# Optimization experiments

Hardware: AMD Instinct MI355X
Metric: run time of the kernel (lower is better)

The kernel has to match this reference:

```python
import jax, jax.numpy as jnp
import numpy as np

B, L, D, H = 2, 2048, 1024, 16
NEG = -1.0e9


def setup_inputs() -> dict:
    key = jax.random.key(0)
    k1, k2, k3, k4 = jax.random.split(key, 4)
    query = jax.random.normal(k1, (B, L, D), dtype=jnp.float32)
    key_t = jax.random.normal(k2, (B, L, D), dtype=jnp.float32)
    value = jax.random.normal(k3, (B, L, D), dtype=jnp.float32)
    # Conv1D c_proj params: w ~ N(0, 0.02), b = 0   (nx=D -> nf=D)
    w_proj = 0.02 * jax.random.normal(k4, (D, D), dtype=jnp.float32)
    b_proj = jnp.zeros((D,), dtype=jnp.float32)
    return {"query": query, "key": key_t, "value": value,
            "w_proj": w_proj, "b_proj": b_proj, "n_head": H}


def reference(query, key, value, w_proj, b_proj, n_head):
    b, l, d = query.shape
    dh = d // n_head
    # split_heads -> [B, H, L, dh]
    q = query.reshape(b, l, n_head, dh).transpose(0, 2, 1, 3)
    k = key.reshape(b, l, n_head, dh).transpose(0, 2, 1, 3)
    v = value.reshape(b, l, n_head, dh).transpose(0, 2, 1, 3)
    # scores: [B, H, L, L], scaled by sqrt(head_dim) (v.size(-1) after split)
    w = jnp.einsum("bhqd,bhkd->bhqk", q, k) / jnp.sqrt(jnp.float32(dh))
    # one_dir_visible=True: multiplicative causal mask, w*m + (-1e9)*(1-m)
    m = jnp.tril(jnp.ones((l, l), dtype=w.dtype))[None, None]
    w = w * m + NEG * (1.0 - m)
    p = jax.nn.softmax(w, axis=-1)  # attn_dropout p=0 -> identity
    a = jnp.einsum("bhqk,bhkd->bhqd", p, v)  # [B, H, L, dh]
    # merge_heads -> [B, L, D]
    a = a.transpose(0, 2, 1, 3).reshape(b, l, d)
    # c_proj (Conv1D == dense): resid_dropout p=0 -> identity
    return a @ w_proj + b_proj
```

## Files before the change

kernel.cpp:

```cpp
#include <hip/hip_runtime.h>
#include <hip/hip_bf16.h>

constexpr int kB  = 2;
constexpr int kL  = 2048;
constexpr int kD  = 1024;
constexpr int kH  = 16;
constexpr int kDH = 64;
constexpr int kM  = kB * kL;

typedef _Float16 half8 __attribute__((ext_vector_type(8)));
typedef float    f32x4 __attribute__((ext_vector_type(4)));

constexpr size_t kKhOff = 0;
constexpr size_t kVtOff = 8388608;
constexpr size_t kAhOff = 16777216;
constexpr size_t kWtOff = 25165824;
constexpr size_t kWsNeed = 27262976;

__device__ __forceinline__ void load16_lds(const void* g, void* l) {
    __builtin_amdgcn_global_load_lds((__attribute__((address_space(1))) void*)(g),
                                     (__attribute__((address_space(3))) void*)(l),
                                     16, 0, 0);
}

__global__ __launch_bounds__(256) void conv_fused(const float* __restrict__ K,
                                                  const float* __restrict__ V,
                                                  const float* __restrict__ W,
                                                  _Float16* __restrict__ Kh,
                                                  _Float16* __restrict__ Vt,
                                                  _Float16* __restrict__ Wt) {
    __shared__ _Float16 Ts[64][65];
    const int t = threadIdx.x;
    const int bid = blockIdx.x;

    if (bid < 2048) {
        size_t i = ((size_t)bid * 256 + t) * 8;
        float4 f0 = *(const float4*)(K + i);
        float4 f1 = *(const float4*)(K + i + 4);
        half8 h;
        h[0] = (_Float16)f0.x; h[1] = (_Float16)f0.y; h[2] = (_Float16)f0.z; h[3] = (_Float16)f0.w;
        h[4] = (_Float16)f1.x; h[5] = (_Float16)f1.y; h[6] = (_Float16)f1.z; h[7] = (_Float16)f1.w;
        *(half8*)(Kh + i) = h;
    } else if (bid < 3072) {
        const int b2 = bid - 2048;
        const int lt = b2 & 31, h = (b2 >> 5) & 15, b = b2 >> 9;
        for (int p = 0; p < 16; ++p) {
            int i = p * 256 + t;
            int r = i >> 6, c = i & 63;
            Ts[r][c] = (_Float16)V[((size_t)(b * kL + lt * 64 + r)) * kD + h * kDH + c];
        }
        __syncthreads();
        for (int p = 0; p < 16; ++p) {
            int i = p * 256 + t;
            int r = i >> 6, c = i & 63;
            Vt[((size_t)(b * kH + h) * kDH + r) * kL + lt * 64 + c] = Ts[c][r];
        }
    } else {
        const int b3 = bid - 3072;
        const int nt = b3 & 15, kt = b3 >> 4;
        const int k0 = kt * 64, n0 = nt * 64;
        for (int p = 0; p < 16; ++p) {
            int i = p * 256 + t;
            int r = i >> 6, c = i & 63;
            Ts[r][c] = (_Float16)W[(size_t)(k0 + r) * kD + n0 + c];
        }
        __syncthreads();
        for (int p = 0; p < 16; ++p) {
            int i = p * 256 + t;
            int r = i >> 6, c = i & 63;
            Wt[(size_t)(n0 + r) * kD + k0 + c] = Ts[c][r];
        }
    }
}

__global__ __launch_bounds__(256, 4) void flash_kernel(const float* __restrict__ Q,
                                                       const _Float16* __restrict__ Kh,
                                                       const _Float16* __restrict__ Vt,
                                                       _Float16* __restrict__ Ah) {
    __shared__ __align__(16) _Float16 Ks[2][64 * 64];
    __shared__ __align__(16) _Float16 Vs[2][64 * 64];
    __shared__ __align__(16) _Float16 Ps[4][16 * 64];

    const int t = threadIdx.x;
    const int lane = t & 63, w = t >> 6;
    const int l15 = lane & 15, quad = lane >> 4;
    const int lhi = l15 >> 3, llo = l15 & 7;
    const int bid = blockIdx.x;
    const int bh = bid & 31;
    const int qt = 31 - (bid >> 5);
    const int b = bh >> 4, h = bh & 15;
    const int Tq = qt + 1;
    const int qrow0 = qt * 64 + w * 16;
    const size_t hoff = (size_t)h * kDH;

    const int srow = w * 16 + (lane >> 3);
    const int sj   = ((lane & 7) - (lane >> 3)) & 7;
    const _Float16* kgp = Kh + (size_t)(b * kL) * kD + hoff + sj * 8;
    const _Float16* vgp = Vt + (size_t)(bh * kDH) * kL + sj * 8;

    half8 aq[2];
    #pragma unroll
    for (int kc = 0; kc < 2; ++kc) {
        const float* qp = Q + (size_t)(b * kL + qrow0 + l15) * kD + hoff + kc * 32 + quad * 8;
        float4 f0 = *(const float4*)qp;
        float4 f1 = *(const float4*)(qp + 4);
        half8 hq;
        hq[0] = (_Float16)(f0.x * 0.125f); hq[1] = (_Float16)(f0.y * 0.125f);
        hq[2] = (_Float16)(f0.z * 0.125f); hq[3] = (_Float16)(f0.w * 0.125f);
        hq[4] = (_Float16)(f1.x * 0.125f); hq[5] = (_Float16)(f1.y * 0.125f);
        hq[6] = (_Float16)(f1.z * 0.125f); hq[7] = (_Float16)(f1.w * 0.125f);
        aq[kc] = hq;
    }

    half8 ones;
    #pragma unroll
    for (int i = 0; i < 8; ++i) ones[i] = (_Float16)1.0f;

    f32x4 o[4];
    f32x4 lsum = (f32x4){0.f, 0.f, 0.f, 0.f};
    #pragma unroll
    for (int nt = 0; nt < 4; ++nt) o[nt] = (f32x4){0.f, 0.f, 0.f, 0.f};

    _Float16* pp = Ps[w];

    constexpr float kLog2e = 1.4426950408889634f;
    constexpr float kBias  = -11.541560327111707f;

    load16_lds(kgp + (size_t)srow * kD,       &Ks[0][(w * 16) * 64]);
    load16_lds(kgp + (size_t)(srow + 8) * kD, &Ks[0][(w * 16 + 8) * 64]);
    load16_lds(vgp + (size_t)srow * kL,       &Vs[0][(w * 16) * 64]);
    load16_lds(vgp + (size_t)(srow + 8) * kL, &Vs[0][(w * 16 + 8) * 64]);

    for (int kt = 0; kt < Tq; ++kt) {
        const int cur = kt & 1;
        __syncthreads();

        if (kt + 1 < Tq) {
            const int kb1 = (kt + 1) * 64;
            load16_lds(kgp + (size_t)(kb1 + srow) * kD,     &Ks[cur ^ 1][(w * 16) * 64]);
            load16_lds(kgp + (size_t)(kb1 + srow + 8) * kD, &Ks[cur ^ 1][(w * 16 + 8) * 64]);
            load16_lds(vgp + (size_t)srow * kL + kb1,       &Vs[cur ^ 1][(w * 16) * 64]);
            load16_lds(vgp + (size_t)(srow + 8) * kL + kb1, &Vs[cur ^ 1][(w * 16 + 8) * 64]);
        }

        f32x4 s[4];
        #pragma unroll
        for (int nt = 0; nt < 4; ++nt) {
            s[nt] = (f32x4){0.f, 0.f, 0.f, 0.f};
            #pragma unroll
            for (int kc = 0; kc < 2; ++kc) {
                const int r = nt * 16 + l15;
                const int slot = (quad + 4 * kc + l15) & 7;
                half8 bk = *(half8*)&Ks[cur][r * 64 + slot * 8];
                s[nt] = __builtin_amdgcn_mfma_f32_16x16x32_f16(aq[kc], bk, s[nt], 0, 0, 0);
            }
        }

        if (kt == Tq - 1) {
            const int kb = kt * 64;
            const int row = qrow0 + quad * 4;
            #pragma unroll
            for (int nt = 0; nt < 4; ++nt)
                #pragma unroll
                for (int r = 0; r < 4; ++r)
                    if (kb + nt * 16 + l15 > row + r) s[nt][r] = -1.0e30f;
        }

        #pragma unroll
        for (int nt = 0; nt < 4; ++nt)
            #pragma unroll
            for (int r = 0; r < 4; ++r) {
                float p = exp2f(fmaf(s[nt][r], kLog2e, kBias));
                const int prow = quad * 4 + r;
                const int slot = (nt * 2 + lhi + prow) & 7;
                pp[prow * 64 + slot * 8 + llo] = (_Float16)p;
            }

        half8 ap[2];
        #pragma unroll
        for (int kc = 0; kc < 2; ++kc) {
            const int slot = (kc * 4 + quad + l15) & 7;
            ap[kc] = *(half8*)&pp[l15 * 64 + slot * 8];
        }

        #pragma unroll
        for (int nt = 0; nt < 4; ++nt)
            #pragma unroll
            for (int kc = 0; kc < 2; ++kc) {
                const int r = nt * 16 + l15;
                const int slot = (quad + 4 * kc + l15) & 7;
                half8 bv = *(half8*)&Vs[cur][r * 64 + slot * 8];
                o[nt] = __builtin_amdgcn_mfma_f32_16x16x32_f16(ap[kc], bv, o[nt], 0, 0, 0);
            }
        lsum = __builtin_amdgcn_mfma_f32_16x16x32_f16(ap[0], ones, lsum, 0, 0, 0);
        lsum = __builtin_amdgcn_mfma_f32_16x16x32_f16(ap[1], ones, lsum, 0, 0, 0);
    }

    const size_t orow = (size_t)(b * kL + qrow0 + quad * 4);
    #pragma unroll
    for (int r = 0; r < 4; ++r) {
        float inv = 1.0f / lsum[r];
        #pragma unroll
        for (int nt = 0; nt < 4; ++nt)
            Ah[(orow + r) * kD + hoff + nt * 16 + l15] = (_Float16)(o[nt][r] * inv);
    }
}

__global__ __launch_bounds__(256, 4) void proj_half(const _Float16* __restrict__ Ah,
                                                    const _Float16* __restrict__ Wt,
                                                    const float* __restrict__ bias,
                                                    float* __restrict__ out) {
    __shared__ __align__(16) _Float16 As[2][64 * 64];
    __shared__ __align__(16) _Float16 Bs[2][64 * 64];

    const int t = threadIdx.x;
    const int lane = t & 63, w = t >> 6;
    const int l15 = lane & 15, quad = lane >> 4;
    const int m0 = blockIdx.x * 64, n0 = blockIdx.y * 64;

    const int srow = w * 16 + (lane >> 3);
    const int sj   = ((lane & 7) - (lane >> 3)) & 7;
    const _Float16* agp = Ah + (size_t)(m0 + srow) * kD + sj * 8;
    const _Float16* bgp = Wt + (size_t)(n0 + srow) * kD + sj * 8;

    f32x4 c[4];
    #pragma unroll
    for (int nt = 0; nt < 4; ++nt) c[nt] = (f32x4){0.f, 0.f, 0.f, 0.f};

    load16_lds(agp,                    &As[0][(w * 16) * 64]);
    load16_lds(agp + (size_t)8 * kD,   &As[0][(w * 16 + 8) * 64]);
    load16_lds(bgp,                    &Bs[0][(w * 16) * 64]);
    load16_lds(bgp + (size_t)8 * kD,   &Bs[0][(w * 16 + 8) * 64]);

    for (int kt = 0; kt < 16; ++kt) {
        const int cur = kt & 1;
        __syncthreads();

        if (kt + 1 < 16) {
            const int k1 = (kt + 1) * 64;
            load16_lds(agp + k1,                  &As[cur ^ 1][(w * 16) * 64]);
            load16_lds(agp + (size_t)8 * kD + k1, &As[cur ^ 1][(w * 16 + 8) * 64]);
            load16_lds(bgp + k1,                  &Bs[cur ^ 1][(w * 16) * 64]);
            load16_lds(bgp + (size_t)8 * kD + k1, &Bs[cur ^ 1][(w * 16 + 8) * 64]);
        }

        #pragma unroll
        for (int kc = 0; kc < 2; ++kc) {
            const int arow = w * 16 + l15;
            const int aslot = (kc * 4 + quad + l15) & 7;
            half8 a = *(half8*)&As[cur][arow * 64 + aslot * 8];
            #pragma unroll
            for (int nt = 0; nt < 4; ++nt) {
                const int brow = nt * 16 + l15;
                const int bslot = (kc * 4 + quad + l15) & 7;
                half8 bf = *(half8*)&Bs[cur][brow * 64 + bslot * 8];
                c[nt] = __builtin_amdgcn_mfma_f32_16x16x32_f16(a, bf, c[nt], 0, 0, 0);
            }
        }
    }

    #pragma unroll
    for (int nt = 0; nt < 4; ++nt) {
        const int n = n0 + nt * 16 + l15;
        const float bv = bias[n];
        const int mrow = m0 + w * 16 + quad * 4;
        #pragma unroll
        for (int r = 0; r < 4; ++r)
            out[(size_t)(mrow + r) * kD + n] = c[nt][r] + bv;
    }
}

__global__ __launch_bounds__(256) void attn_kernel_f32(const float* __restrict__ Q,
                                                       const float* __restrict__ K,
                                                       const float* __restrict__ V,
                                                       float* __restrict__ A) {
    const int lane = threadIdx.x & 63;
    const int wave = threadIdx.x >> 6;
    const int tilesPerBH = kL / 4;
    const int bh = blockIdx.x / tilesPerBH;
    const int tile = blockIdx.x % tilesPerBH;
    const int b = bh / kH, h = bh % kH;
    const int qi = tile * 4 + wave;
    const size_t base = (size_t)b * kL * kD + (size_t)h * kDH;
    const float* kptr = K + base;
    const float* vptr = V + base;
    const float qd = Q[base + (size_t)qi * kD + lane] * 0.125f;
    float m = -3.0e38f, l = 0.0f, acc = 0.0f;
    for (int j = 0; j <= qi; ++j) {
        const float kd = kptr[(size_t)j * kD + lane];
        float s = qd * kd;
        #pragma unroll
        for (int off = 32; off; off >>= 1) s += __shfl_xor(s, off);
        const float mnew = fmaxf(m, s);
        const float corr = __expf(m - mnew);
        const float p = __expf(s - mnew);
        const float vd = vptr[(size_t)j * kD + lane];
        l = l * corr + p;
        acc = acc * corr + p * vd;
        m = mnew;
    }
    A[base + (size_t)qi * kD + lane] = acc / l;
}

__global__ __launch_bounds__(256) void proj_kernel_f32(const float* __restrict__ A,
                                                       const float* __restrict__ W,
                                                       const float* __restrict__ bias,
                                                       float* __restrict__ out) {
    __shared__ __align__(16) float As[16][64];
    __shared__ __align__(16) float Ws[16][64];
    const int t = threadIdx.x;
    const int m0 = blockIdx.x * 64, n0 = blockIdx.y * 64;
    const int tx = t & 15, ty = t >> 4;
    const int arow = t >> 2, acol4 = (t & 3) * 4;
    const int wrow = t >> 4, wcol4 = (t & 15) * 4;
    float c[4][4] = {};
    for (int k0 = 0; k0 < kD; k0 += 16) {
        const float4 av = *(const float4*)(A + (size_t)(m0 + arow) * kD + k0 + acol4);
        const float4 wv = *(const float4*)(W + (size_t)(k0 + wrow) * kD + n0 + wcol4);
        __syncthreads();
        As[acol4 + 0][arow] = av.x;
        As[acol4 + 1][arow] = av.y;
        As[acol4 + 2][arow] = av.z;
        As[acol4 + 3][arow] = av.w;
        *(float4*)&Ws[wrow][wcol4] = wv;
        __syncthreads();
        #pragma unroll
        for (int kk = 0; kk < 16; ++kk) {
            const float4 a = *(const float4*)&As[kk][ty * 4];
            const float4 wv2 = *(const float4*)&Ws[kk][tx * 4];
            c[0][0] += a.x * wv2.x; c[0][1] += a.x * wv2.y; c[0][2] += a.x * wv2.z; c[0][3] += a.x * wv2.w;
            c[1][0] += a.y * wv2.x; c[1][1] += a.y * wv2.y; c[1][2] += a.y * wv2.z; c[1][3] += a.y * wv2.w;
            c[2][0] += a.z * wv2.x; c[2][1] += a.z * wv2.y; c[2][2] += a.z * wv2.z; c[2][3] += a.z * wv2.w;
            c[3][0] += a.w * wv2.x; c[3][1] += a.w * wv2.y; c[3][2] += a.w * wv2.z; c[3][3] += a.w * wv2.w;
        }
    }
    const float4 bv = *(const float4*)(bias + n0 + tx * 4);
    #pragma unroll
    for (int i = 0; i < 4; ++i) {
        float4 o;
        o.x = c[i][0] + bv.x; o.y = c[i][1] + bv.y; o.z = c[i][2] + bv.z; o.w = c[i][3] + bv.w;
        *(float4*)(out + (size_t)(m0 + ty * 4 + i) * kD + n0 + tx * 4) = o;
    }
}

extern "C" void kernel_launch(void* const* d_in, const int* in_sizes, int n_in,
                              void* d_out, int out_size, void* d_ws, size_t ws_size,
                              hipStream_t stream) {
    const float* Q    = (const float*)d_in[0];
    const float* K    = (const float*)d_in[1];
    const float* V    = (const float*)d_in[2];
    const float* W    = (const float*)d_in[3];
    const float* bias = (const float*)d_in[4];
    float* out = (float*)d_out;

    if (ws_size >= kWsNeed) {
        char* ws = (char*)d_ws;
        _Float16* Kh = (_Float16*)(ws + kKhOff);
        _Float16* Vt = (_Float16*)(ws + kVtOff);
        _Float16* Ah = (_Float16*)(ws + kAhOff);
        _Float16* Wt = (_Float16*)(ws + kWtOff);

        conv_fused<<<dim3(3328), 256, 0, stream>>>(K, V, W, Kh, Vt, Wt);
        flash_kernel<<<dim3(1024), 256, 0, stream>>>(Q, Kh, Vt, Ah);
        proj_half<<<dim3(kM / 64, kD / 64), 256, 0, stream>>>(Ah, Wt, bias, out);
    } else {
        float* A = (float*)d_ws;
        attn_kernel_f32<<<dim3(kB * kH * (kL / 4)), 256, 0, stream>>>(Q, K, V, A);
        proj_kernel_f32<<<dim3(kM / 64, kD / 64), 256, 0, stream>>>(A, W, bias, out);
    }
}
```

Baseline: 157.1 us.

## Give each flash-attention wave 32 query rows and reorder causal tile scheduling

The flash kernel now uses 2 waves of 128 threads instead of 4, and each wave owns 32 query rows as two 16-row groups. Every K/V fragment read from LDS therefore feeds two MFMAs, halving LDS traffic per MFMA. Query tiles are now assigned in a zigzag order to balance causal work across the grid. The exp is rewritten as __expf(s-8), and register pressure roughly doubles per wave, which lowers occupancy per block.

```diff
diff --git a/kernel.cpp b/kernel.cpp
--- a/kernel.cpp
+++ b/kernel.cpp
@@ -73,136 +73,173 @@
     }
 }
 
-__global__ __launch_bounds__(256, 4) void flash_kernel(const float* __restrict__ Q,
+__global__ __launch_bounds__(128, 2) void flash_kernel(const float* __restrict__ Q,
                                                        const _Float16* __restrict__ Kh,
                                                        const _Float16* __restrict__ Vt,
                                                        _Float16* __restrict__ Ah) {
     __shared__ __align__(16) _Float16 Ks[2][64 * 64];
     __shared__ __align__(16) _Float16 Vs[2][64 * 64];
-    __shared__ __align__(16) _Float16 Ps[4][16 * 64];
+    __shared__ __align__(16) _Float16 Ps[2][32 * 64];
 
     const int t = threadIdx.x;
     const int lane = t & 63, w = t >> 6;
     const int l15 = lane & 15, quad = lane >> 4;
     const int lhi = l15 >> 3, llo = l15 & 7;
+
     const int bid = blockIdx.x;
     const int bh = bid & 31;
-    const int qt = 31 - (bid >> 5);
+    const int j  = (bid >> 5) & 7;
+    const int k4 = bid >> 8;
+    int qt;
+    if      (k4 == 0) qt = 31 - j;
+    else if (k4 == 1) qt = 16 + j;
+    else if (k4 == 2) qt = 15 - j;
+    else              qt = j;
+
     const int b = bh >> 4, h = bh & 15;
     const int Tq = qt + 1;
-    const int qrow0 = qt * 64 + w * 16;
+    const int qrow0 = qt * 64 + w * 32;
     const size_t hoff = (size_t)h * kDH;
 
-    const int srow = w * 16 + (lane >> 3);
+    const int srow = w * 32 + (lane >> 3);
     const int sj   = ((lane & 7) - (lane >> 3)) & 7;
     const _Float16* kgp = Kh + (size_t)(b * kL) * kD + hoff + sj * 8;
     const _Float16* vgp = Vt + (size_t)(bh * kDH) * kL + sj * 8;
-
-    half8 aq[2];
-    #pragma unroll
-    for (int kc = 0; kc < 2; ++kc) {
-        const float* qp = Q + (size_t)(b * kL + qrow0 + l15) * kD + hoff + kc * 32 + quad * 8;
-        float4 f0 = *(const float4*)qp;
-        float4 f1 = *(const float4*)(qp + 4);
-        half8 hq;
-        hq[0] = (_Float16)(f0.x * 0.125f); hq[1] = (_Float16)(f0.y * 0.125f);
-        hq[2] = (_Float16)(f0.z * 0.125f); hq[3] = (_Float16)(f0.w * 0.125f);
-        hq[4] = (_Float16)(f1.x * 0.125f); hq[5] = (_Float16)(f1.y * 0.125f);
-        hq[6] = (_Float16)(f1.z * 0.125f); hq[7] = (_Float16)(f1.w * 0.125f);
-        aq[kc] = hq;
-    }
+    const _Float16* kp = kgp + (size_t)srow * kD;
+    const _Float16* vp = vgp + (size_t)srow * kL;
+
+    half8 aq[2][2];
+    #pragma unroll
+    for (int rg = 0; rg < 2; ++rg)
+        #pragma unroll
+        for (int kc = 0; kc < 2; ++kc) {
+            const float* qp = Q + (size_t)(b * kL + qrow0 + rg * 16 + l15) * kD + hoff + kc * 32 + quad * 8;
+            float4 f0 = *(const float4*)qp;
+            float4 f1 = *(const float4*)(qp + 4);
+            half8 hq;
+            hq[0] = (_Float16)(f0.x * 0.125f); hq[1] = (_Float16)(f0.y * 0.125f);
+            hq[2] = (_Float16)(f0.z * 0.125f); hq[3] = (_Float16)(f0.w * 0.125f);
+            hq[4] = (_Float16)(f1.x * 0.125f); hq[5] = (_Float16)(f1.y * 0.125f);
+            hq[6] = (_Float16)(f1.z * 0.125f); hq[7] = (_Float16)(f1.w * 0.125f);
+            aq[rg][kc] = hq;
+        }
 
     half8 ones;
     #pragma unroll
     for (int i = 0; i < 8; ++i) ones[i] = (_Float16)1.0f;
 
-    f32x4 o[4];
-    f32x4 lsum = (f32x4){0.f, 0.f, 0.f, 0.f};
-    #pragma unroll
-    for (int nt = 0; nt < 4; ++nt) o[nt] = (f32x4){0.f, 0.f, 0.f, 0.f};
+    f32x4 o[2][4];
+    f32x4 lsum[2];
+    #pragma unroll
+    for (int rg = 0; rg < 2; ++rg) {
+        lsum[rg] = (f32x4){0.f, 0.f, 0.f, 0.f};
+        #pragma unroll
+        for (int nt = 0; nt < 4; ++nt) o[rg][nt] = (f32x4){0.f, 0.f, 0.f, 0.f};
+    }
 
     _Float16* pp = Ps[w];
 
-    constexpr float kLog2e = 1.4426950408889634f;
-    constexpr float kBias  = -11.541560327111707f;
-
-    load16_lds(kgp + (size_t)srow * kD,       &Ks[0][(w * 16) * 64]);
-    load16_lds(kgp + (size_t)(srow + 8) * kD, &Ks[0][(w * 16 + 8) * 64]);
-    load16_lds(vgp + (size_t)srow * kL,       &Vs[0][(w * 16) * 64]);
-    load16_lds(vgp + (size_t)(srow + 8) * kL, &Vs[0][(w * 16 + 8) * 64]);
+    auto stage = [&](int buf, const _Float16* kp_, const _Float16* vp_) {
+        load16_lds(kp_,                   &Ks[buf][(w * 32 +  0) * 64]);
+        load16_lds(kp_ + (size_t) 8 * kD, &Ks[buf][(w * 32 +  8) * 64]);
+        load16_lds(kp_ + (size_t)16 * kD, &Ks[buf][(w * 32 + 16) * 64]);
+        load16_lds(kp_ + (size_t)24 * kD, &Ks[buf][(w * 32 + 24) * 64]);
+        load16_lds(vp_,                   &Vs[buf][(w * 32 +  0) * 64]);
+        load16_lds(vp_ + (size_t) 8 * kL, &Vs[buf][(w * 32 +  8) * 64]);
+        load16_lds(vp_ + (size_t)16 * kL, &Vs[buf][(w * 32 + 16) * 64]);
+        load16_lds(vp_ + (size_t)24 * kL, &Vs[buf][(w * 32 + 24) * 64]);
+    };
+
+    stage(0, kp, vp);
+    const _Float16* kpn = kp + (size_t)64 * kD;
+    const _Float16* vpn = vp + 64;
 
     for (int kt = 0; kt < Tq; ++kt) {
         const int cur = kt & 1;
         __syncthreads();
 
         if (kt + 1 < Tq) {
-            const int kb1 = (kt + 1) * 64;
-            load16_lds(kgp + (size_t)(kb1 + srow) * kD,     &Ks[cur ^ 1][(w * 16) * 64]);
-            load16_lds(kgp + (size_t)(kb1 + srow + 8) * kD, &Ks[cur ^ 1][(w * 16 + 8) * 64]);
-            load16_lds(vgp + (size_t)srow * kL + kb1,       &Vs[cur ^ 1][(w * 16) * 64]);
-            load16_lds(vgp + (size_t)(srow + 8) * kL + kb1, &Vs[cur ^ 1][(w * 16 + 8) * 64]);
-        }
-
-        f32x4 s[4];
-        #pragma unroll
-        for (int nt = 0; nt < 4; ++nt) {
-            s[nt] = (f32x4){0.f, 0.f, 0.f, 0.f};
-            #pragma unroll
-            for (int kc = 0; kc < 2; ++kc) {
-                const int r = nt * 16 + l15;
-                const int slot = (quad + 4 * kc + l15) & 7;
-                half8 bk = *(half8*)&Ks[cur][r * 64 + slot * 8];
-                s[nt] = __builtin_amdgcn_mfma_f32_16x16x32_f16(aq[kc], bk, s[nt], 0, 0, 0);
+            stage(cur ^ 1, kpn, vpn);
+            kpn += (size_t)64 * kD;
+            vpn += 64;
+        }
+
+        f32x4 s[2][4];
+        #pragma unroll
+        for (int rg = 0; rg < 2; ++rg)
+            #pragma unroll
+            for (int nt = 0; nt < 4; ++nt) s[rg][nt] = (f32x4){0.f, 0.f, 0.f, 0.f};
+
+        #pragma unroll
+        for (int kc = 0; kc < 2; ++kc)
+            #pragma unroll
+            for (int nt = 0; nt < 4; ++nt) {
+                const int slot = (kc * 4 + quad + l15) & 7;
+                half8 bk = *(half8*)&Ks[cur][(nt * 16 + l15) * 64 + slot * 8];
+                s[0][nt] = __builtin_amdgcn_mfma_f32_16x16x32_f16(aq[0][kc], bk, s[0][nt], 0, 0, 0);
+                s[1][nt] = __builtin_amdgcn_mfma_f32_16x16x32_f16(aq[1][kc], bk, s[1][nt], 0, 0, 0);
             }
-        }
 
         if (kt == Tq - 1) {
             const int kb = kt * 64;
-            const int row = qrow0 + quad * 4;
+            #pragma unroll
+            for (int rg = 0; rg < 2; ++rg) {
+                const int row = qrow0 + rg * 16 + quad * 4;
+                #pragma unroll
+                for (int nt = 0; nt < 4; ++nt)
+                    #pragma unroll
+                    for (int r = 0; r < 4; ++r)
+                        if (kb + nt * 16 + l15 > row + r) s[rg][nt][r] = -1.0e30f;
+            }
+        }
+
+        #pragma unroll
+        for (int rg = 0; rg < 2; ++rg)
             #pragma unroll
             for (int nt = 0; nt < 4; ++nt)
                 #pragma unroll
-                for (int r = 0; r < 4; ++r)
-                    if (kb + nt * 16 + l15 > row + r) s[nt][r] = -1.0e30f;
-        }
+                for (int r = 0; r < 4; ++r) {
+                    float p = __expf(s[rg][nt][r] - 8.0f);
+                    const int prow = rg * 16 + quad * 4 + r;
+                    const int slot = (nt * 2 + lhi + prow) & 7;
+                    pp[prow * 64 + slot * 8 + llo] = (_Float16)p;
+                }
+
+        half8 ap[2][2];
+        #pragma unroll
+        for (int rg = 0; rg < 2; ++rg)
+            #pragma unroll
+            for (int kc = 0; kc < 2; ++kc) {
+                const int slot = (kc * 4 + quad + l15) & 7;
+                ap[rg][kc] = *(half8*)&pp[(rg * 16 + l15) * 64 + slot * 8];
+            }
 
         #pragma unroll
         for (int nt = 0; nt < 4; ++nt)
             #pragma unroll
-            for (int r = 0; r < 4; ++r) {
-                float p = exp2f(fmaf(s[nt][r], kLog2e, kBias));
-                const int prow = quad * 4 + r;
-                const int slot = (nt * 2 + lhi + prow) & 7;
-                pp[prow * 64 + slot * 8 + llo] = (_Float16)p;
+            for (int kc = 0; kc < 2; ++kc) {
+                const int slot = (kc * 4 + quad + l15) & 7;
+                half8 bv = *(half8*)&Vs[cur][(nt * 16 + l15) * 64 + slot * 8];
+                o[0][nt] = __builtin_amdgcn_mfma_f32_16x16x32_f16(ap[0][kc], bv, o[0][nt], 0, 0, 0);
+                o[1][nt] = __builtin_amdgcn_mfma_f32_16x16x32_f16(ap[1][kc], bv, o[1][nt], 0, 0, 0);
             }
-
-        half8 ap[2];
-        #pragma unroll
-        for (int kc = 0; kc < 2; ++kc) {
-            const int slot = (kc * 4 + quad + l15) & 7;
-            ap[kc] = *(half8*)&pp[l15 * 64 + slot * 8];
-        }
-
-        #pragma unroll
-        for (int nt = 0; nt < 4; ++nt)
-            #pragma unroll
-            for (int kc = 0; kc < 2; ++kc) {
-                const int r = nt * 16 + l15;
-                const int slot = (quad + 4 * kc + l15) & 7;
-                half8 bv = *(half8*)&Vs[cur][r * 64 + slot * 8];
-                o[nt] = __builtin_amdgcn_mfma_f32_16x16x32_f16(ap[kc], bv, o[nt], 0, 0, 0);
-            }
-        lsum = __builtin_amdgcn_mfma_f32_16x16x32_f16(ap[0], ones, lsum, 0, 0, 0);
-        lsum = __builtin_amdgcn_mfma_f32_16x16x32_f16(ap[1], ones, lsum, 0, 0, 0);
-    }
-
-    const size_t orow = (size_t)(b * kL + qrow0 + quad * 4);
-    #pragma unroll
-    for (int r = 0; r < 4; ++r) {
-        float inv = 1.0f / lsum[r];
-        #pragma unroll
-        for (int nt = 0; nt < 4; ++nt)
-            Ah[(orow + r) * kD + hoff + nt * 16 + l15] = (_Float16)(o[nt][r] * inv);
+        #pragma unroll
+        for (int rg = 0; rg < 2; ++rg) {
+            lsum[rg] = __builtin_amdgcn_mfma_f32_16x16x32_f16(ap[rg][0], ones, lsum[rg], 0, 0, 0);
+            lsum[rg] = __builtin_amdgcn_mfma_f32_16x16x32_f16(ap[rg][1], ones, lsum[rg], 0, 0, 0);
+        }
+    }
+
+    #pragma unroll
+    for (int rg = 0; rg < 2; ++rg) {
+        const size_t orow = (size_t)(b * kL + qrow0 + rg * 16 + quad * 4);
+        #pragma unroll
+        for (int r = 0; r < 4; ++r) {
+            float inv = 1.0f / lsum[rg][r];
+            #pragma unroll
+            for (int nt = 0; nt < 4; ++nt)
+                Ah[(orow + r) * kD + hoff + nt * 16 + l15] = (_Float16)(o[rg][nt][r] * inv);
+        }
     }
 }
 
@@ -361,7 +398,7 @@
         _Float16* Wt = (_Float16*)(ws + kWtOff);
 
         conv_fused<<<dim3(3328), 256, 0, stream>>>(K, V, W, Kh, Vt, Wt);
-        flash_kernel<<<dim3(1024), 256, 0, stream>>>(Q, Kh, Vt, Ah);
+        flash_kernel<<<dim3(1024), 128, 0, stream>>>(Q, Kh, Vt, Ah);
         proj_half<<<dim3(kM / 64, kD / 64), 256, 0, stream>>>(Ah, Wt, bias, out);
     } else {
         float* A = (float*)d_ws;
```

Measured after the change: 163.7 us. 1.04x slower.

## Load K/V fragments directly from global into registers, drop LDS staging

Applied to the files above, without the earlier changes.

Removes the shared-memory double buffers for K and V in the flash attention kernel. Each wave now loads its MFMA operand fragments for K and V straight from global memory (relying on L2/L1 reuse across the four waves), and keeps a per-iteration barrier. It also remaps block-to-query-tile order to interleave long and short causal rows for load balance, and replaces the exp2 fma with __expf(s-8). The cost is four times as many global loads across waves and the loss of async prefetch overlap, traded against lower LDS use and less LDS traffic.

```diff
diff --git a/kernel.cpp b/kernel.cpp
--- a/kernel.cpp
+++ b/kernel.cpp
@@ -77,26 +77,30 @@
                                                        const _Float16* __restrict__ Kh,
                                                        const _Float16* __restrict__ Vt,
                                                        _Float16* __restrict__ Ah) {
-    __shared__ __align__(16) _Float16 Ks[2][64 * 64];
-    __shared__ __align__(16) _Float16 Vs[2][64 * 64];
     __shared__ __align__(16) _Float16 Ps[4][16 * 64];
 
     const int t = threadIdx.x;
     const int lane = t & 63, w = t >> 6;
     const int l15 = lane & 15, quad = lane >> 4;
     const int lhi = l15 >> 3, llo = l15 & 7;
+
     const int bid = blockIdx.x;
     const int bh = bid & 31;
-    const int qt = 31 - (bid >> 5);
+    const int j  = (bid >> 5) & 7;
+    const int k4 = bid >> 8;
+    int qt;
+    if      (k4 == 0) qt = 31 - j;
+    else if (k4 == 1) qt = 16 + j;
+    else if (k4 == 2) qt = 15 - j;
+    else              qt = j;
+
     const int b = bh >> 4, h = bh & 15;
     const int Tq = qt + 1;
     const int qrow0 = qt * 64 + w * 16;
     const size_t hoff = (size_t)h * kDH;
 
-    const int srow = w * 16 + (lane >> 3);
-    const int sj   = ((lane & 7) - (lane >> 3)) & 7;
-    const _Float16* kgp = Kh + (size_t)(b * kL) * kD + hoff + sj * 8;
-    const _Float16* vgp = Vt + (size_t)(bh * kDH) * kL + sj * 8;
+    const _Float16* kfp = Kh + ((size_t)(b * kL) + l15) * kD + hoff + quad * 8;
+    const _Float16* vfp = Vt + ((size_t)(bh * kDH) + l15) * kL + quad * 8;
 
     half8 aq[2];
     #pragma unroll
@@ -123,41 +127,37 @@
 
     _Float16* pp = Ps[w];
 
-    constexpr float kLog2e = 1.4426950408889634f;
-    constexpr float kBias  = -11.541560327111707f;
-
-    load16_lds(kgp + (size_t)srow * kD,       &Ks[0][(w * 16) * 64]);
-    load16_lds(kgp + (size_t)(srow + 8) * kD, &Ks[0][(w * 16 + 8) * 64]);
-    load16_lds(vgp + (size_t)srow * kL,       &Vs[0][(w * 16) * 64]);
-    load16_lds(vgp + (size_t)(srow + 8) * kL, &Vs[0][(w * 16 + 8) * 64]);
-
     for (int kt = 0; kt < Tq; ++kt) {
-        const int cur = kt & 1;
-        __syncthreads();
-
-        if (kt + 1 < Tq) {
-            const int kb1 = (kt + 1) * 64;
-            load16_lds(kgp + (size_t)(kb1 + srow) * kD,     &Ks[cur ^ 1][(w * 16) * 64]);
-            load16_lds(kgp + (size_t)(kb1 + srow + 8) * kD, &Ks[cur ^ 1][(w * 16 + 8) * 64]);
-            load16_lds(vgp + (size_t)srow * kL + kb1,       &Vs[cur ^ 1][(w * 16) * 64]);
-            load16_lds(vgp + (size_t)(srow + 8) * kL + kb1, &Vs[cur ^ 1][(w * 16 + 8) * 64]);
-        }
+        const int kb = kt * 64;
+        __builtin_amdgcn_s_barrier();
+
+        const _Float16* kq = kfp + (size_t)kb * kD;
+        const _Float16* vq = vfp + kb;
+
+        half8 kf[2][4];
+        #pragma unroll
+        for (int kc = 0; kc < 2; ++kc)
+            #pragma unroll
+            for (int nt = 0; nt < 4; ++nt)
+                kf[kc][nt] = *(const half8*)(kq + (size_t)(nt * 16) * kD + kc * 32);
 
         f32x4 s[4];
         #pragma unroll
         for (int nt = 0; nt < 4; ++nt) {
             s[nt] = (f32x4){0.f, 0.f, 0.f, 0.f};
             #pragma unroll
-            for (int kc = 0; kc < 2; ++kc) {
-                const int r = nt * 16 + l15;
-                const int slot = (quad + 4 * kc + l15) & 7;
-                half8 bk = *(half8*)&Ks[cur][r * 64 + slot * 8];
-                s[nt] = __builtin_amdgcn_mfma_f32_16x16x32_f16(aq[kc], bk, s[nt], 0, 0, 0);
-            }
-        }
+            for (int kc = 0; kc < 2; ++kc)
+                s[nt] = __builtin_amdgcn_mfma_f32_16x16x32_f16(aq[kc], kf[kc][nt], s[nt], 0, 0, 0);
+        }
+
+        half8 vf[2][4];
+        #pragma unroll
+        for (int kc = 0; kc < 2; ++kc)
+            #pragma unroll
+            for (int nt = 0; nt < 4; ++nt)
+                vf[kc][nt] = *(const half8*)(vq + (size_t)(nt * 16) * kL + kc * 32);
 
         if (kt == Tq - 1) {
-            const int kb = kt * 64;
             const int row = qrow0 + quad * 4;
             #pragma unroll
             for (int nt = 0; nt < 4; ++nt)
@@ -170,7 +170,7 @@
         for (int nt = 0; nt < 4; ++nt)
             #pragma unroll
             for (int r = 0; r < 4; ++r) {
-                float p = exp2f(fmaf(s[nt][r], kLog2e, kBias));
+                float p = __expf(s[nt][r] - 8.0f);
                 const int prow = quad * 4 + r;
                 const int slot = (nt * 2 + lhi + prow) & 7;
                 pp[prow * 64 + slot * 8 + llo] = (_Float16)p;
@@ -186,12 +186,8 @@
         #pragma unroll
         for (int nt = 0; nt < 4; ++nt)
             #pragma unroll
-            for (int kc = 0; kc < 2; ++kc) {
-                const int r = nt * 16 + l15;
-                const int slot = (quad + 4 * kc + l15) & 7;
-                half8 bv = *(half8*)&Vs[cur][r * 64 + slot * 8];
-                o[nt] = __builtin_amdgcn_mfma_f32_16x16x32_f16(ap[kc], bv, o[nt], 0, 0, 0);
-            }
+            for (int kc = 0; kc < 2; ++kc)
+                o[nt] = __builtin_amdgcn_mfma_f32_16x16x32_f16(ap[kc], vf[kc][nt], o[nt], 0, 0, 0);
         lsum = __builtin_amdgcn_mfma_f32_16x16x32_f16(ap[0], ones, lsum, 0, 0, 0);
         lsum = __builtin_amdgcn_mfma_f32_16x16x32_f16(ap[1], ones, lsum, 0, 0, 0);
     }
```

Result: slower. 251.7 us (+60.2%).
